# Optimization experiments

Measured on AMD Instinct MI355X. Metric: run time of the kernel, lower is better.

## Reference

```python
import jax, jax.numpy as jnp
import numpy as np
import math

P = 256   # state_dim
H = 1024  # hidden_dim
B = 8     # batch
L = 4096  # sequence length
R_MIN, R_MAX, THETA_MAX = 0.9, 0.999, math.pi


def _map_theta_to_A(thetas, G_diag, steps):
    cos_t = jnp.cos(thetas)
    tan_sq = jnp.tan(thetas) ** 2
    sqrt_term = 4.0 * jnp.sqrt(steps ** 4 / cos_t ** 2 + steps ** 5 * G_diag / cos_t ** 2)
    common = steps ** 2 * (-4.0 - 2.0 * steps * G_diag - 4.0 * tan_sq - 2.0 * steps * G_diag * tan_sq)
    denom = 2.0 * steps ** 4 * (1.0 + tan_sq)
    A_plus = (sqrt_term - common) / denom
    A_minus = (-sqrt_term - common) / denom
    return jnp.where(thetas > math.pi / 2, A_plus, A_minus)


def setup_inputs() -> dict:
    key = jax.random.key(0)
    k1, k2, k3, k4, k5, k6, k7 = jax.random.split(key, 7)
    x = jax.random.normal(k1, (B, L, H), dtype=jnp.float32)
    steps_raw = 0.5 * jax.random.normal(k2, (P,), dtype=jnp.float32)
    steps = jax.nn.sigmoid(steps_raw)
    mags = jnp.sqrt(jax.random.uniform(k3, (P,)) * (R_MAX ** 2 - R_MIN ** 2) + R_MIN ** 2)
    G_raw = (1.0 - mags ** 2) / (steps * mags ** 2)
    theta = jax.random.uniform(k4, (P,)) * THETA_MAX
    A_raw = _map_theta_to_A(theta, jax.nn.relu(G_raw), steps)
    std_b = 1.0 / math.sqrt(H)
    B_mat = jax.random.uniform(k5, (P, H, 2), minval=-std_b, maxval=std_b, dtype=jnp.float32)
    std_c = 1.0 / math.sqrt(P)
    C_mat = jax.random.uniform(k6, (H, P, 2), minval=-std_c, maxval=std_c, dtype=jnp.float32)
    D_vec = jax.random.normal(k7, (H,), dtype=jnp.float32)
    return {"input_sequence": x, "steps_raw": steps_raw, "G_raw": G_raw,
            "A_raw": A_raw, "B_mat": B_mat, "C_mat": C_mat, "D_vec": D_vec}


def _binary_operator(q_i, q_j):
    """Compose (M, F) pairs: (Mj@Mi, Mj@Fi + Fj); M flattened as [M11,M12,M21,M22] (4P)."""
    A_i, b_i = q_i
    A_j, b_j = q_j
    iA, iB, iC, iD = jnp.split(A_i, 4, axis=-1)
    jA, jB, jC, jD = jnp.split(A_j, 4, axis=-1)
    A_new = jnp.concatenate([jA * iA + jB * iC, jA * iB + jB * iD,
                             jC * iA + jD * iC, jC * iB + jD * iD], axis=-1)
    b_i1, b_i2 = jnp.split(b_i, 2, axis=-2)  # (..., P, 2) each
    new_b1 = jA[..., None] * b_i1 + jB[..., None] * b_i2
    new_b2 = jC[..., None] * b_i1 + jD[..., None] * b_i2
    return A_new, jnp.concatenate([new_b1, new_b2], axis=-2) + b_j


def _forward(x, steps_raw, G_raw, A_raw, B_mat, C_mat, D_vec):
    steps = jax.nn.sigmoid(steps_raw)          # (P,)
    G_diag = jax.nn.relu(G_raw)
    A_diag = jax.nn.relu(A_raw)

    Bu = jnp.einsum('blh,pht->blpt', x, B_mat)  # (B, L, P, 2)

    S = 1.0 + steps * G_diag                    # (P,)
    alpha = steps ** 2 * A_diag / S
    alpha = 1.99 * jnp.tanh(alpha / 1.99)
    M = jnp.concatenate([1.0 / S, -alpha / steps, steps / S, 1.0 - alpha])  # (4P,)
    M_exp = jnp.broadcast_to(M, (x.shape[0], x.shape[1], 4 * steps.shape[0]))

    step_b = steps[None, None, :, None]
    S_b = S[None, None, :, None]
    F1 = step_b * (1.0 / S_b) * Bu
    F2 = step_b ** 2 * (1.0 / S_b) * Bu
    F_mat = jnp.concatenate([F1, F2], axis=-2)  # (B, L, 2P, 2)

    _, xs = jax.lax.associative_scan(_binary_operator, (M_exp, F_mat), axis=1)
    ys = xs[..., steps.shape[0]:, :]            # (B, L, P, 2) -- the x-states

    Cy = jnp.einsum('blpt,hpt->blht', ys, C_mat)  # (B, L, H, 2)
    return Cy[..., 0] - Cy[..., 1] + x * D_vec


def reference(input_sequence, steps_raw, G_raw, A_raw, B_mat, C_mat, D_vec):
    return _forward(input_sequence, steps_raw, G_raw, A_raw, B_mat, C_mat, D_vec)
```

## Files before the change

kernel.cpp:

```cpp
#include <hip/hip_runtime.h>
#include <math.h>
#include <stdint.h>

#define PCH 256
#define HD  1024
#define BB  8
#define LL  4096
#define NN  512
#define MROWS (BB*LL)
#define NCH 64
#define TCH 64

typedef __bf16 bf16x8 __attribute__((ext_vector_type(8)));
typedef float  f32x4  __attribute__((ext_vector_type(4)));
typedef short  s16x8  __attribute__((ext_vector_type(8)));

#define OFFB_W1    ((size_t)0)
#define OFFB_C2    (OFFB_W1  + (size_t)NN*HD*2)
#define OFFB_CST   (OFFB_C2  + (size_t)HD*NN*2)
#define OFFB_BU    (OFFB_CST + (size_t)16384)
#define OFFB_YS    (OFFB_BU  + (size_t)MROWS*NN*2)
#define OFFB_ZEND  (OFFB_YS  + (size_t)MROWS*NN*2)
#define OFFB_CARRY (OFFB_ZEND + (size_t)BB*NCH*2*NN*4)

__device__ __forceinline__ short f2bf(float f) {
    union { float f; uint32_t u; } v; v.f = f;
    uint32_t r = v.u + 0x7FFFu + ((v.u >> 16) & 1u);
    return (short)(r >> 16);
}
__device__ __forceinline__ float bf2f(unsigned short u) {
    union { uint32_t u; float f; } v; v.u = ((uint32_t)u) << 16;
    return v.f;
}

__global__ void prep_consts(const float* __restrict__ steps_raw,
                            const float* __restrict__ G_raw,
                            const float* __restrict__ A_raw,
                            float* __restrict__ cst) {
    int p = threadIdx.x;
    if (p >= PCH) return;
    float steps = 1.0f / (1.0f + expf(-steps_raw[p]));
    float G = fmaxf(G_raw[p], 0.0f);
    float A = fmaxf(A_raw[p], 0.0f);
    float S = 1.0f + steps * G;
    float alpha = steps * steps * A / S;
    alpha = 1.99f * tanhf(alpha / 1.99f);
    float m11 = 1.0f / S;
    float m12 = -alpha / steps;
    float m21 = steps / S;
    float m22 = 1.0f - alpha;
    float c1 = steps / S;
    float c2 = steps * steps / S;
    float a = 1.f, b = 0.f, c = 0.f, d = 1.f;
    for (int i = 0; i < TCH; ++i) {
        float na = m11*a + m12*c;
        float nb = m11*b + m12*d;
        float nc = m21*a + m22*c;
        float nd = m21*b + m22*d;
        a = na; b = nb; c = nc; d = nd;
    }
    cst[0*PCH+p] = m11; cst[1*PCH+p] = m12; cst[2*PCH+p] = m21; cst[3*PCH+p] = m22;
    cst[4*PCH+p] = c1;  cst[5*PCH+p] = c2;
    cst[6*PCH+p] = a;   cst[7*PCH+p] = b;   cst[8*PCH+p] = c;   cst[9*PCH+p] = d;
}

__global__ void prep_w(const float* __restrict__ B_mat,
                       const float* __restrict__ C_mat,
                       short* __restrict__ W1t,
                       short* __restrict__ C2t) {
    int idx = blockIdx.x * blockDim.x + threadIdx.x;
    if (idx >= HD * NN) return;
    {
        int n = idx >> 10;
        int h = idx & (HD - 1);
        int p = n >> 1, t = n & 1;
        W1t[idx] = f2bf(B_mat[(size_t)p * HD * 2 + (size_t)h * 2 + t]);
    }
    {
        int h = idx >> 9;
        int n = idx & (NN - 1);
        int p = n >> 1, t = n & 1;
        float sgn = (t == 0) ? 1.0f : -1.0f;
        C2t[idx] = f2bf(sgn * C_mat[(size_t)h * PCH * 2 + (size_t)p * 2 + t]);
    }
}

template <int K, int N>
__global__ __launch_bounds__(512, 2)
void gemm256_cvtA(const float* __restrict__ Af32, const short* __restrict__ Bt,
                  unsigned short* __restrict__ Cout) {
    __shared__ alignas(16) char smem[131072];
    constexpr int GX = N / 256;
    const int nwg = gridDim.x;
    const int cpx = nwg >> 3;
    const int bid = blockIdx.x;
    const int wg = (bid & 7) * cpx + (bid >> 3);
    const int by = wg / GX, bx = wg % GX;
    const int m0 = by * 256, n0 = bx * 256;

    const int tid = threadIdx.x;
    const int lane = tid & 63, w = tid >> 6;
    const int wm = w >> 2, wn = w & 3;
    const int g = lane >> 4, r16 = lane & 15;

    auto stageB = [&](int buf, int k0) {
        #pragma unroll
        for (int s = 0; s < 4; ++s) {
            int c = tid + s * 512;
            int row = c >> 3, q = c & 7;
            int gq = q ^ (row & 7);
            const short* sb = Bt + (size_t)(n0 + row) * K + k0 + gq * 8;
            __builtin_amdgcn_global_load_lds(
                (const __attribute__((address_space(1))) void*)sb,
                (__attribute__((address_space(3))) void*)(smem + buf * 65536 + 32768 + c * 16),
                16, 0, 0);
        }
    };
    f32x4 av[4][2];
    auto loadA = [&](int k0) {
        #pragma unroll
        for (int s = 0; s < 4; ++s) {
            int c = tid + s * 512;
            int row = c >> 3, q = c & 7;
            int gq = q ^ (row & 7);
            const f32x4* px = (const f32x4*)(Af32 + (size_t)(m0 + row) * K + k0 + gq * 8);
            av[s][0] = px[0]; av[s][1] = px[1];
        }
    };
    auto writeA = [&](int buf) {
        #pragma unroll
        for (int s = 0; s < 4; ++s) {
            int c = tid + s * 512;
            int row = c >> 3, q = c & 7;
            s16x8 r;
            #pragma unroll
            for (int j = 0; j < 4; ++j) { r[j] = f2bf(av[s][0][j]); r[4 + j] = f2bf(av[s][1][j]); }
            *(s16x8*)(smem + buf * 65536 + row * 128 + q * 16) = r;
        }
    };

    int aoff[8], boff[4];
    #pragma unroll
    for (int mi = 0; mi < 8; ++mi) {
        int ra = wm * 128 + mi * 16 + r16;
        aoff[mi] = ra * 128 + ((g ^ (ra & 7)) << 4);
    }
    #pragma unroll
    for (int nj = 0; nj < 4; ++nj) {
        int rb = wn * 64 + nj * 16 + r16;
        boff[nj] = 32768 + rb * 128 + ((g ^ (rb & 7)) << 4);
    }

    f32x4 acc[8][4];
    #pragma unroll
    for (int mi = 0; mi < 8; ++mi)
        #pragma unroll
        for (int nj = 0; nj < 4; ++nj) acc[mi][nj] = (f32x4)0.0f;

    constexpr int NT = K / 64;
    loadA(0); stageB(0, 0); writeA(0);
    __syncthreads();
    int cur = 0;
    #pragma unroll 1
    for (int t = 0; t < NT; ++t) {
        if (t + 1 < NT) {
            loadA((t + 1) * 64);
            stageB(cur ^ 1, (t + 1) * 64);
        }
        const char* base = smem + cur * 65536;
        #pragma unroll
        for (int kk = 0; kk < 2; ++kk) {
            bf16x8 af[8], bfv[4];
            #pragma unroll
            for (int mi = 0; mi < 8; ++mi)
                af[mi] = *(const bf16x8*)(base + (aoff[mi] ^ (kk << 6)));
            #pragma unroll
            for (int nj = 0; nj < 4; ++nj)
                bfv[nj] = *(const bf16x8*)(base + (boff[nj] ^ (kk << 6)));
            #pragma unroll
            for (int mi = 0; mi < 8; ++mi)
                #pragma unroll
                for (int nj = 0; nj < 4; ++nj)
                    acc[mi][nj] = __builtin_amdgcn_mfma_f32_16x16x32_bf16(
                        af[mi], bfv[nj], acc[mi][nj], 0, 0, 0);
        }
        if (t + 1 < NT) writeA(cur ^ 1);
        __syncthreads();
        cur ^= 1;
    }

    const int crow0 = m0 + wm * 128 + g * 4;
    const int ccol0 = n0 + wn * 64 + r16;
    #pragma unroll
    for (int nj = 0; nj < 4; ++nj) {
        int col = ccol0 + nj * 16;
        #pragma unroll
        for (int mi = 0; mi < 8; ++mi) {
            #pragma unroll
            for (int r = 0; r < 4; ++r) {
                size_t idx = (size_t)(crow0 + mi * 16 + r) * N + col;
                Cout[idx] = (unsigned short)f2bf(acc[mi][nj][r]);
            }
        }
    }
}

template <int K, int N, bool EPI>
__global__ __launch_bounds__(512, 2)
void gemm256(const short* __restrict__ A, const short* __restrict__ Bt,
             float* __restrict__ Cout, const float* __restrict__ xres,
             const float* __restrict__ Dv) {
    __shared__ alignas(16) char smem[131072];
    constexpr int GX = N / 256;
    const int nwg = gridDim.x;
    const int cpx = nwg >> 3;
    const int bid = blockIdx.x;
    const int wg = (bid & 7) * cpx + (bid >> 3);
    const int by = wg / GX, bx = wg % GX;
    const int m0 = by * 256, n0 = bx * 256;

    const int tid = threadIdx.x;
    const int lane = tid & 63, w = tid >> 6;
    const int wm = w >> 2, wn = w & 3;
    const int g = lane >> 4, r16 = lane & 15;

    auto stage = [&](int buf, int k0) {
        #pragma unroll
        for (int s = 0; s < 4; ++s) {
            int c = tid + s * 512;
            int row = c >> 3, q = c & 7;
            int gq = q ^ (row & 7);
            const short* sa = A + (size_t)(m0 + row) * K + k0 + gq * 8;
            __builtin_amdgcn_global_load_lds(
                (const __attribute__((address_space(1))) void*)sa,
                (__attribute__((address_space(3))) void*)(smem + buf * 65536 + c * 16),
                16, 0, 0);
        }
        #pragma unroll
        for (int s = 0; s < 4; ++s) {
            int c = tid + s * 512;
            int row = c >> 3, q = c & 7;
            int gq = q ^ (row & 7);
            const short* sb = Bt + (size_t)(n0 + row) * K + k0 + gq * 8;
            __builtin_amdgcn_global_load_lds(
                (const __attribute__((address_space(1))) void*)sb,
                (__attribute__((address_space(3))) void*)(smem + buf * 65536 + 32768 + c * 16),
                16, 0, 0);
        }
    };

    int aoff[8], boff[4];
    #pragma unroll
    for (int mi = 0; mi < 8; ++mi) {
        int ra = wm * 128 + mi * 16 + r16;
        aoff[mi] = ra * 128 + ((g ^ (ra & 7)) << 4);
    }
    #pragma unroll
    for (int nj = 0; nj < 4; ++nj) {
        int rb = wn * 64 + nj * 16 + r16;
        boff[nj] = 32768 + rb * 128 + ((g ^ (rb & 7)) << 4);
    }

    f32x4 acc[8][4];
    #pragma unroll
    for (int mi = 0; mi < 8; ++mi)
        #pragma unroll
        for (int nj = 0; nj < 4; ++nj) acc[mi][nj] = (f32x4)0.0f;

    constexpr int NT = K / 64;
    stage(0, 0);
    __syncthreads();
    int cur = 0;
    #pragma unroll 1
    for (int t = 0; t < NT; ++t) {
        if (t + 1 < NT) stage(cur ^ 1, (t + 1) * 64);
        const char* base = smem + cur * 65536;
        #pragma unroll
        for (int kk = 0; kk < 2; ++kk) {
            bf16x8 af[8], bfv[4];
            #pragma unroll
            for (int mi = 0; mi < 8; ++mi)
                af[mi] = *(const bf16x8*)(base + (aoff[mi] ^ (kk << 6)));
            #pragma unroll
            for (int nj = 0; nj < 4; ++nj)
                bfv[nj] = *(const bf16x8*)(base + (boff[nj] ^ (kk << 6)));
            #pragma unroll
            for (int mi = 0; mi < 8; ++mi)
                #pragma unroll
                for (int nj = 0; nj < 4; ++nj)
                    acc[mi][nj] = __builtin_amdgcn_mfma_f32_16x16x32_bf16(
                        af[mi], bfv[nj], acc[mi][nj], 0, 0, 0);
        }
        __syncthreads();
        cur ^= 1;
    }

    const int crow0 = m0 + wm * 128 + g * 4;
    const int ccol0 = n0 + wn * 64 + r16;
    #pragma unroll
    for (int nj = 0; nj < 4; ++nj) {
        int col = ccol0 + nj * 16;
        float dv = EPI ? Dv[col] : 0.0f;
        #pragma unroll
        for (int mi = 0; mi < 8; ++mi) {
            #pragma unroll
            for (int r = 0; r < 4; ++r) {
                size_t idx = (size_t)(crow0 + mi * 16 + r) * N + col;
                float v = acc[mi][nj][r];
                if (EPI) v = fmaf(xres[idx], dv, v);
                Cout[idx] = v;
            }
        }
    }
}

__global__ __launch_bounds__(512)
void scan_phase1(const unsigned short* __restrict__ Bu, const float* __restrict__ cst,
                 float* __restrict__ zend) {
    int bid = blockIdx.x;
    int b = bid / NCH, c = bid % NCH;
    int n = threadIdx.x;
    int p = n >> 1;
    float m11 = cst[0*PCH+p], m12 = cst[1*PCH+p], m21 = cst[2*PCH+p], m22 = cst[3*PCH+p];
    float c1 = cst[4*PCH+p], c2 = cst[5*PCH+p];
    float s1 = 0.f, s2 = 0.f;
    const unsigned short* bp = Bu + ((size_t)(b * LL + c * TCH)) * NN + n;
    #pragma unroll 4
    for (int i = 0; i < TCH; ++i) {
        float u = bf2f(bp[(size_t)i * NN]);
        float ns1 = fmaf(m11, s1, fmaf(m12, s2, c1 * u));
        float ns2 = fmaf(m21, s1, fmaf(m22, s2, c2 * u));
        s1 = ns1; s2 = ns2;
    }
    size_t base = ((size_t)(b * NCH + c) * 2) * NN + n;
    zend[base] = s1;
    zend[base + NN] = s2;
}

__global__ __launch_bounds__(512)
void scan_phase2(const float* __restrict__ zend, const float* __restrict__ cst,
                 float* __restrict__ carry) {
    int b = blockIdx.x;
    int n = threadIdx.x;
    int p = n >> 1;
    float a = cst[6*PCH+p], bm = cst[7*PCH+p], cmt = cst[8*PCH+p], d = cst[9*PCH+p];
    float cs1 = 0.f, cs2 = 0.f;
    for (int c = 0; c < NCH; ++c) {
        size_t base = ((size_t)(b * NCH + c) * 2) * NN + n;
        float z1 = zend[base], z2 = zend[base + NN];
        float ns1 = fmaf(a, cs1, fmaf(bm, cs2, z1));
        float ns2 = fmaf(cmt, cs1, fmaf(d, cs2, z2));
        carry[base] = ns1;
        carry[base + NN] = ns2;
        cs1 = ns1; cs2 = ns2;
    }
}

__global__ __launch_bounds__(512)
void scan_phase3(const unsigned short* __restrict__ Bu, const float* __restrict__ cst,
                 const float* __restrict__ carry, unsigned short* __restrict__ ys) {
    int bid = blockIdx.x;
    int b = bid / NCH, c = bid % NCH;
    int n = threadIdx.x;
    int p = n >> 1;
    float m11 = cst[0*PCH+p], m12 = cst[1*PCH+p], m21 = cst[2*PCH+p], m22 = cst[3*PCH+p];
    float c1 = cst[4*PCH+p], c2 = cst[5*PCH+p];
    float s1 = 0.f, s2 = 0.f;
    if (c > 0) {
        size_t base = ((size_t)(b * NCH + (c - 1)) * 2) * NN + n;
        s1 = carry[base];
        s2 = carry[base + NN];
    }
    const unsigned short* bp = Bu + ((size_t)(b * LL + c * TCH)) * NN + n;
    unsigned short* yp = ys + ((size_t)(b * LL + c * TCH)) * NN + n;
    #pragma unroll 4
    for (int i = 0; i < TCH; ++i) {
        float u = bf2f(bp[(size_t)i * NN]);
        float ns1 = fmaf(m11, s1, fmaf(m12, s2, c1 * u));
        float ns2 = fmaf(m21, s1, fmaf(m22, s2, c2 * u));
        s1 = ns1; s2 = ns2;
        yp[(size_t)i * NN] = (unsigned short)f2bf(s2);
    }
}

extern "C" void kernel_launch(void* const* d_in, const int* in_sizes, int n_in,
                              void* d_out, int out_size, void* d_ws, size_t ws_size,
                              hipStream_t stream) {
    const float* x         = (const float*)d_in[0];
    const float* steps_raw = (const float*)d_in[1];
    const float* G_raw     = (const float*)d_in[2];
    const float* A_raw     = (const float*)d_in[3];
    const float* B_mat     = (const float*)d_in[4];
    const float* C_mat     = (const float*)d_in[5];
    const float* D_vec     = (const float*)d_in[6];
    float* out = (float*)d_out;
    char*  ws  = (char*)d_ws;

    short*          W1t   = (short*)(ws + OFFB_W1);
    short*          C2t   = (short*)(ws + OFFB_C2);
    float*          cst   = (float*)(ws + OFFB_CST);
    unsigned short* Bu    = (unsigned short*)(ws + OFFB_BU);
    unsigned short* ysbf  = (unsigned short*)(ws + OFFB_YS);
    float*          zend  = (float*)(ws + OFFB_ZEND);
    float*          carry = (float*)(ws + OFFB_CARRY);

    prep_consts<<<1, 256, 0, stream>>>(steps_raw, G_raw, A_raw, cst);
    prep_w<<<(HD * NN) / 512, 512, 0, stream>>>(B_mat, C_mat, W1t, C2t);

    gemm256_cvtA<HD, NN><<<(NN / 256) * (MROWS / 256), 512, 0, stream>>>(
        x, W1t, Bu);

    scan_phase1<<<BB * NCH, 512, 0, stream>>>(Bu, cst, zend);
    scan_phase2<<<BB, 512, 0, stream>>>(zend, cst, carry);
    scan_phase3<<<BB * NCH, 512, 0, stream>>>(Bu, cst, carry, ysbf);

    gemm256<NN, HD, true><<<(HD / 256) * (MROWS / 256), 512, 0, stream>>>(
        (const short*)ysbf, C2t, out, x, D_vec);
}
```

Baseline: 180.6 us.

## Fuse scan phase-1 into first GEMM epilogue and register-stage A in second GEMM

The first GEMM now computes per-chunk scan end states directly after writing its Bu tile. It re-reads the just-written bf16 Bu from global memory, where it is likely still cached, and so removes the separate scan_phase1 launch and its extra pass over Bu. The second GEMM switches its A operand from async global_load_lds to loads into registers followed by LDS writes after the MFMA loop, so A loads overlap compute differently. The fused scan adds a serial 64-step tail per block and relies on __syncthreads being enough for visibility of the block's own global writes.

```diff
diff --git a/kernel.cpp b/kernel.cpp
--- a/kernel.cpp
+++ b/kernel.cpp
@@ -87,8 +87,9 @@
 
 template <int K, int N>
 __global__ __launch_bounds__(512, 2)
-void gemm256_cvtA(const float* __restrict__ Af32, const short* __restrict__ Bt,
-                  unsigned short* __restrict__ Cout) {
+void gemm1_cvtA_p1(const float* __restrict__ Af32, const short* __restrict__ Bt,
+                   unsigned short* __restrict__ Bu, const float* __restrict__ cst,
+                   float* __restrict__ zend) {
     __shared__ alignas(16) char smem[131072];
     constexpr int GX = N / 256;
     const int nwg = gridDim.x;
@@ -199,17 +200,43 @@
             #pragma unroll
             for (int r = 0; r < 4; ++r) {
                 size_t idx = (size_t)(crow0 + mi * 16 + r) * N + col;
-                Cout[idx] = (unsigned short)f2bf(acc[mi][nj][r]);
+                Bu[idx] = (unsigned short)f2bf(acc[mi][nj][r]);
             }
         }
+    }
+
+    __syncthreads();
+    const int b  = m0 >> 12;
+    const int c0 = (m0 & (LL - 1)) >> 6;
+    #pragma unroll 1
+    for (int pass = 0; pass < 2; ++pass) {
+        int s = tid + pass * 512;
+        int col = s & 255, cc = s >> 8;
+        int n = n0 + col;
+        int p = n >> 1;
+        float m11 = cst[0*PCH+p], m12 = cst[1*PCH+p];
+        float m21 = cst[2*PCH+p], m22 = cst[3*PCH+p];
+        float c1 = cst[4*PCH+p], c2 = cst[5*PCH+p];
+        float s1 = 0.f, s2 = 0.f;
+        const unsigned short* bp = Bu + (size_t)(m0 + cc * TCH) * N + n;
+        #pragma unroll 4
+        for (int i = 0; i < TCH; ++i) {
+            float u = bf2f(bp[(size_t)i * N]);
+            float ns1 = fmaf(m11, s1, fmaf(m12, s2, c1 * u));
+            float ns2 = fmaf(m21, s1, fmaf(m22, s2, c2 * u));
+            s1 = ns1; s2 = ns2;
+        }
+        size_t zb = ((size_t)((b * NCH + (c0 + cc)) * 2)) * NN + n;
+        zend[zb] = s1;
+        zend[zb + NN] = s2;
     }
 }
 
 template <int K, int N, bool EPI>
 __global__ __launch_bounds__(512, 2)
-void gemm256(const short* __restrict__ A, const short* __restrict__ Bt,
-             float* __restrict__ Cout, const float* __restrict__ xres,
-             const float* __restrict__ Dv) {
+void gemm2_regA(const unsigned short* __restrict__ A, const short* __restrict__ Bt,
+                float* __restrict__ Cout, const float* __restrict__ xres,
+                const float* __restrict__ Dv) {
     __shared__ alignas(16) char smem[131072];
     constexpr int GX = N / 256;
     const int nwg = gridDim.x;
@@ -224,18 +251,7 @@
     const int wm = w >> 2, wn = w & 3;
     const int g = lane >> 4, r16 = lane & 15;
 
-    auto stage = [&](int buf, int k0) {
-        #pragma unroll
-        for (int s = 0; s < 4; ++s) {
-            int c = tid + s * 512;
-            int row = c >> 3, q = c & 7;
-            int gq = q ^ (row & 7);
-            const short* sa = A + (size_t)(m0 + row) * K + k0 + gq * 8;
-            __builtin_amdgcn_global_load_lds(
-                (const __attribute__((address_space(1))) void*)sa,
-                (__attribute__((address_space(3))) void*)(smem + buf * 65536 + c * 16),
-                16, 0, 0);
-        }
+    auto stageB = [&](int buf, int k0) {
         #pragma unroll
         for (int s = 0; s < 4; ++s) {
             int c = tid + s * 512;
@@ -248,6 +264,24 @@
                 16, 0, 0);
         }
     };
+    s16x8 av[4];
+    auto loadA = [&](int k0) {
+        #pragma unroll
+        for (int s = 0; s < 4; ++s) {
+            int c = tid + s * 512;
+            int row = c >> 3, q = c & 7;
+            int gq = q ^ (row & 7);
+            av[s] = *(const s16x8*)(A + (size_t)(m0 + row) * K + k0 + gq * 8);
+        }
+    };
+    auto writeA = [&](int buf) {
+        #pragma unroll
+        for (int s = 0; s < 4; ++s) {
+            int c = tid + s * 512;
+            int row = c >> 3, q = c & 7;
+            *(s16x8*)(smem + buf * 65536 + row * 128 + q * 16) = av[s];
+        }
+    };
 
     int aoff[8], boff[4];
     #pragma unroll
@@ -268,12 +302,15 @@
         for (int nj = 0; nj < 4; ++nj) acc[mi][nj] = (f32x4)0.0f;
 
     constexpr int NT = K / 64;
-    stage(0, 0);
+    loadA(0); stageB(0, 0); writeA(0);
     __syncthreads();
     int cur = 0;
     #pragma unroll 1
     for (int t = 0; t < NT; ++t) {
-        if (t + 1 < NT) stage(cur ^ 1, (t + 1) * 64);
+        if (t + 1 < NT) {
+            loadA((t + 1) * 64);
+            stageB(cur ^ 1, (t + 1) * 64);
+        }
         const char* base = smem + cur * 65536;
         #pragma unroll
         for (int kk = 0; kk < 2; ++kk) {
@@ -291,6 +328,7 @@
                     acc[mi][nj] = __builtin_amdgcn_mfma_f32_16x16x32_bf16(
                         af[mi], bfv[nj], acc[mi][nj], 0, 0, 0);
         }
+        if (t + 1 < NT) writeA(cur ^ 1);
         __syncthreads();
         cur ^= 1;
     }
@@ -312,29 +350,6 @@
             }
         }
     }
-}
-
-__global__ __launch_bounds__(512)
-void scan_phase1(const unsigned short* __restrict__ Bu, const float* __restrict__ cst,
-                 float* __restrict__ zend) {
-    int bid = blockIdx.x;
-    int b = bid / NCH, c = bid % NCH;
-    int n = threadIdx.x;
-    int p = n >> 1;
-    float m11 = cst[0*PCH+p], m12 = cst[1*PCH+p], m21 = cst[2*PCH+p], m22 = cst[3*PCH+p];
-    float c1 = cst[4*PCH+p], c2 = cst[5*PCH+p];
-    float s1 = 0.f, s2 = 0.f;
-    const unsigned short* bp = Bu + ((size_t)(b * LL + c * TCH)) * NN + n;
-    #pragma unroll 4
-    for (int i = 0; i < TCH; ++i) {
-        float u = bf2f(bp[(size_t)i * NN]);
-        float ns1 = fmaf(m11, s1, fmaf(m12, s2, c1 * u));
-        float ns2 = fmaf(m21, s1, fmaf(m22, s2, c2 * u));
-        s1 = ns1; s2 = ns2;
-    }
-    size_t base = ((size_t)(b * NCH + c) * 2) * NN + n;
-    zend[base] = s1;
-    zend[base + NN] = s2;
 }
 
 __global__ __launch_bounds__(512)
@@ -407,13 +422,12 @@
     prep_consts<<<1, 256, 0, stream>>>(steps_raw, G_raw, A_raw, cst);
     prep_w<<<(HD * NN) / 512, 512, 0, stream>>>(B_mat, C_mat, W1t, C2t);
 
-    gemm256_cvtA<HD, NN><<<(NN / 256) * (MROWS / 256), 512, 0, stream>>>(
-        x, W1t, Bu);
-
-    scan_phase1<<<BB * NCH, 512, 0, stream>>>(Bu, cst, zend);
+    gemm1_cvtA_p1<HD, NN><<<(NN / 256) * (MROWS / 256), 512, 0, stream>>>(
+        x, W1t, Bu, cst, zend);
+
     scan_phase2<<<BB, 512, 0, stream>>>(zend, cst, carry);
     scan_phase3<<<BB * NCH, 512, 0, stream>>>(Bu, cst, carry, ysbf);
 
-    gemm256<NN, HD, true><<<(HD / 256) * (MROWS / 256), 512, 0, stream>>>(
-        (const short*)ysbf, C2t, out, x, D_vec);
-}
+    gemm2_regA<NN, HD, true><<<(HD / 256) * (MROWS / 256), 512, 0, stream>>>(
+        ysbf, C2t, out, x, D_vec);
+}
```

Result: slower. 188.0 us (+4.1%).
